# Optimization experiments

Measured on AMD Instinct MI355X. Metric: run time of the kernel, lower is better.

The kernel has to match this reference:

```python
import jax, jax.numpy as jnp
import numpy as np

N_NODES = 50000
N_EDGES = 800000
N_GRAPHS = 512
HEADS = 4
HDIM = 64
NEG_SLOPE = 0.2


def setup_inputs() -> dict:
    key = jax.random.key(0)
    ks = jax.random.split(key, 16)
    x = jax.random.normal(ks[0], (N_NODES, 128), dtype=jnp.float32)
    edge_index = jax.random.randint(ks[1], (2, N_EDGES), 0, N_NODES, dtype=jnp.int64)
    batch = jnp.sort(jax.random.randint(ks[2], (N_NODES,), 0, N_GRAPHS, dtype=jnp.int64))
    def glorot(k, shape):
        fan = shape[0] + shape[-1]
        return jax.random.normal(k, shape, dtype=jnp.float32) * jnp.sqrt(2.0 / fan)
    return {
        "x": x, "edge_index": edge_index, "batch": batch,
        "W1": glorot(ks[3], (128, 256)), "a_src1": glorot(ks[4], (HEADS, HDIM)), "a_dst1": glorot(ks[5], (HEADS, HDIM)), "b1": jnp.zeros((256,), jnp.float32),
        "W2": glorot(ks[6], (256, 256)), "a_src2": glorot(ks[7], (HEADS, HDIM)), "a_dst2": glorot(ks[8], (HEADS, HDIM)), "b2": jnp.zeros((256,), jnp.float32),
        "W3": glorot(ks[9], (256, 256)), "a_src3": glorot(ks[10], (HEADS, HDIM)), "a_dst3": glorot(ks[11], (HEADS, HDIM)), "b3": jnp.zeros((256,), jnp.float32),
        "fc_W": glorot(ks[12], (256, 1)), "fc_b": jnp.zeros((1,), jnp.float32),
    }


def gat_layer(x, W, a_src, a_dst, b, src, dst):
    # x: [N, F_in] -> h: [N, H, C]
    N = x.shape[0]
    h = (x @ W).reshape(N, HEADS, HDIM)
    alpha_s = jnp.sum(h * a_src[None], axis=-1)  # [N, H]
    alpha_d = jnp.sum(h * a_dst[None], axis=-1)  # [N, H]
    logits = jax.nn.leaky_relu(alpha_s[src] + alpha_d[dst], NEG_SLOPE)  # [E, H]
    # segment softmax over destination nodes
    m = jax.ops.segment_max(logits, dst, num_segments=N)  # [N, H]
    e = jnp.exp(logits - m[dst])
    denom = jax.ops.segment_sum(e, dst, num_segments=N)
    alpha = e / denom[dst]  # [E, H]
    msg = h[src] * alpha[:, :, None]  # [E, H, C]
    out = jax.ops.segment_sum(msg, dst, num_segments=N).reshape(N, HEADS * HDIM)
    return out + b


def reference(x, edge_index, batch, W1, a_src1, a_dst1, b1, W2, a_src2, a_dst2, b2, W3, a_src3, a_dst3, b3, fc_W, fc_b):
    N = x.shape[0]
    loop = jnp.arange(N, dtype=edge_index.dtype)
    # PyG GATConv adds self-loops by default
    src = jnp.concatenate([edge_index[0], loop])
    dst = jnp.concatenate([edge_index[1], loop])
    h = gat_layer(x, W1, a_src1, a_dst1, b1, src, dst)
    h = gat_layer(h, W2, a_src2, a_dst2, b2, src, dst)
    h = gat_layer(h, W3, a_src3, a_dst3, b3, src, dst)
    pooled = jax.ops.segment_sum(h, batch, num_segments=N_GRAPHS)  # [G, 256]
    return pooled @ fc_W + fc_b
```

## Files before the change

### kernel.cpp

```cpp
#include <hip/hip_runtime.h>
#include <hip/hip_bf16.h>
#include <math.h>

#define NN 50000
#define NE 800000
#define ET (NE + NN)
#define NG 512
#define NEG 0.2f

typedef __attribute__((ext_vector_type(8))) short bf16x8;
typedef __attribute__((ext_vector_type(4))) float f32x4;

__device__ inline unsigned f2o(float f) {
    unsigned b = __float_as_uint(f);
    return (b & 0x80000000u) ? ~b : (b | 0x80000000u);
}
__device__ inline float o2f(unsigned u) {
    return (u & 0x80000000u) ? __uint_as_float(u ^ 0x80000000u) : __uint_as_float(~u);
}
__device__ inline unsigned short f2b(float f) {
    unsigned u = __float_as_uint(f);
    u += 0x7fffu + ((u >> 16) & 1u);
    return (unsigned short)(u >> 16);
}
__device__ inline float b2f(unsigned short b) {
    return __uint_as_float(((unsigned)b) << 16);
}

__global__ __launch_bounds__(256) void split_weights(const float* __restrict__ W1,
        const float* __restrict__ W2, const float* __restrict__ W3,
        unsigned short* __restrict__ WTh, unsigned short* __restrict__ WTl) {
    int tid = blockIdx.x * 256 + threadIdx.x;
    const float* W; int K, n, k, base;
    if (tid < 32768)       { W = W1; K = 128; base = 0;     int i = tid;          n = i >> 7; k = i & 127; }
    else if (tid < 98304)  { W = W2; K = 256; base = 32768; int i = tid - 32768;  n = i >> 8; k = i & 255; }
    else if (tid < 163840) { W = W3; K = 256; base = 98304; int i = tid - 98304;  n = i >> 8; k = i & 255; }
    else return;
    float w = W[k * 256 + n];
    unsigned short hi = f2b(w);
    float lo = w - b2f(hi);
    WTh[base + n * K + k] = hi;
    WTl[base + n * K + k] = f2b(lo);
}

template<int K, int AFP32>
__global__ __launch_bounds__(256) void gemm_mfma(const float* __restrict__ Af,
        const unsigned short* __restrict__ Ahi, const unsigned short* __restrict__ Alo,
        const unsigned short* __restrict__ Bhi, const unsigned short* __restrict__ Blo,
        unsigned short* __restrict__ h,
        const float* __restrict__ a_src, const float* __restrict__ a_dst,
        float* __restrict__ as_, float* __restrict__ ad_) {
    __shared__ unsigned short AsH[128][40], AsL[128][40], BsH[128][40], BsL[128][40];
    const int t = threadIdx.x;
    const int mb = blockIdx.x >> 1, nb = blockIdx.x & 1;
    const int m0 = mb * 128, n0 = nb * 128;
    const int wid = t >> 6, lane = t & 63;
    const int wr = wid >> 1, wc = wid & 1;
    const int lr = lane & 15, lg = lane >> 4;

    f32x4 acc[4][4];
    #pragma unroll
    for (int mi = 0; mi < 4; ++mi)
        #pragma unroll
        for (int ni = 0; ni < 4; ++ni)
            acc[mi][ni] = (f32x4){0.f, 0.f, 0.f, 0.f};

    for (int k0 = 0; k0 < K; k0 += 32) {
        __syncthreads();
        #pragma unroll
        for (int cc = 0; cc < 2; ++cc) {
            int c = t + cc * 256;
            int row = c >> 2, kc = c & 3;
            int gr = m0 + row; if (gr >= NN) gr = NN - 1;
            if (AFP32) {
                const float* pa = Af + (size_t)gr * K + k0 + kc * 8;
                float4 f0 = *(const float4*)pa;
                float4 f1 = *(const float4*)(pa + 4);
                union { unsigned short u[8]; uint4 v; } th, tl;
                float fs[8] = {f0.x, f0.y, f0.z, f0.w, f1.x, f1.y, f1.z, f1.w};
                #pragma unroll
                for (int j = 0; j < 8; ++j) {
                    unsigned short hv = f2b(fs[j]);
                    th.u[j] = hv;
                    tl.u[j] = f2b(fs[j] - b2f(hv));
                }
                *(uint4*)&AsH[row][kc * 8] = th.v;
                *(uint4*)&AsL[row][kc * 8] = tl.v;
            } else {
                *(uint4*)&AsH[row][kc * 8] = *(const uint4*)(Ahi + (size_t)gr * K + k0 + kc * 8);
                *(uint4*)&AsL[row][kc * 8] = *(const uint4*)(Alo + (size_t)gr * K + k0 + kc * 8);
            }
            *(uint4*)&BsH[row][kc * 8] = *(const uint4*)(Bhi + (size_t)(n0 + row) * K + k0 + kc * 8);
            *(uint4*)&BsL[row][kc * 8] = *(const uint4*)(Blo + (size_t)(n0 + row) * K + k0 + kc * 8);
        }
        __syncthreads();

        bf16x8 ah[4], al[4];
        #pragma unroll
        for (int mi = 0; mi < 4; ++mi) {
            int ra = wr * 64 + mi * 16 + lr;
            ah[mi] = *(const bf16x8*)&AsH[ra][lg * 8];
            al[mi] = *(const bf16x8*)&AsL[ra][lg * 8];
        }
        #pragma unroll
        for (int ni = 0; ni < 4; ++ni) {
            int rb = wc * 64 + ni * 16 + lr;
            bf16x8 bh = *(const bf16x8*)&BsH[rb][lg * 8];
            bf16x8 bl = *(const bf16x8*)&BsL[rb][lg * 8];
            #pragma unroll
            for (int mi = 0; mi < 4; ++mi) {
                acc[mi][ni] = __builtin_amdgcn_mfma_f32_16x16x32_bf16(bh, ah[mi], acc[mi][ni], 0, 0, 0);
                acc[mi][ni] = __builtin_amdgcn_mfma_f32_16x16x32_bf16(bh, al[mi], acc[mi][ni], 0, 0, 0);
                acc[mi][ni] = __builtin_amdgcn_mfma_f32_16x16x32_bf16(bl, ah[mi], acc[mi][ni], 0, 0, 0);
            }
        }
    }

    const int head = nb * 2 + wc;
    const int ncol0 = n0 + wc * 64;
    float4 asv[4], adv[4];
    #pragma unroll
    for (int ni = 0; ni < 4; ++ni) {
        asv[ni] = *(const float4*)&a_src[head * 64 + ni * 16 + lg * 4];
        adv[ni] = *(const float4*)&a_dst[head * 64 + ni * 16 + lg * 4];
    }
    #pragma unroll
    for (int mi = 0; mi < 4; ++mi) {
        float ps = 0.f, pd = 0.f;
        #pragma unroll
        for (int ni = 0; ni < 4; ++ni) {
            ps = fmaf(acc[mi][ni][0], asv[ni].x, ps); pd = fmaf(acc[mi][ni][0], adv[ni].x, pd);
            ps = fmaf(acc[mi][ni][1], asv[ni].y, ps); pd = fmaf(acc[mi][ni][1], adv[ni].y, pd);
            ps = fmaf(acc[mi][ni][2], asv[ni].z, ps); pd = fmaf(acc[mi][ni][2], adv[ni].z, pd);
            ps = fmaf(acc[mi][ni][3], asv[ni].w, ps); pd = fmaf(acc[mi][ni][3], adv[ni].w, pd);
        }
        ps += __shfl_xor(ps, 16, 64); ps += __shfl_xor(ps, 32, 64);
        pd += __shfl_xor(pd, 16, 64); pd += __shfl_xor(pd, 32, 64);
        int row = m0 + wr * 64 + mi * 16 + lr;
        if (row < NN) {
            #pragma unroll
            for (int ni = 0; ni < 4; ++ni) {
                ushort4 hv = {f2b(acc[mi][ni][0]), f2b(acc[mi][ni][1]),
                              f2b(acc[mi][ni][2]), f2b(acc[mi][ni][3])};
                *(ushort4*)&h[(size_t)row * 256 + ncol0 + ni * 16 + lg * 4] = hv;
            }
            if (lane < 16) { as_[row * 4 + head] = ps; ad_[row * 4 + head] = pd; }
        }
    }
}

__global__ void gmax_init(unsigned* gmax) {
    if (threadIdx.x < 4) gmax[threadIdx.x] = 0u;
}
__global__ __launch_bounds__(256) void gmax_reduce(const float* __restrict__ as_,
                                                   unsigned* gmax) {
    float m0 = -1e30f, m1 = -1e30f, m2 = -1e30f, m3 = -1e30f;
    for (int n = blockIdx.x * 256 + threadIdx.x; n < NN; n += gridDim.x * 256) {
        float4 a = *(const float4*)&as_[n * 4];
        m0 = fmaxf(m0, a.x); m1 = fmaxf(m1, a.y);
        m2 = fmaxf(m2, a.z); m3 = fmaxf(m3, a.w);
    }
    #pragma unroll
    for (int off = 32; off; off >>= 1) {
        m0 = fmaxf(m0, __shfl_xor(m0, off, 64));
        m1 = fmaxf(m1, __shfl_xor(m1, off, 64));
        m2 = fmaxf(m2, __shfl_xor(m2, off, 64));
        m3 = fmaxf(m3, __shfl_xor(m3, off, 64));
    }
    __shared__ float sm[4][4];
    int lane = threadIdx.x & 63, w = threadIdx.x >> 6;
    if (lane == 0) { sm[w][0] = m0; sm[w][1] = m1; sm[w][2] = m2; sm[w][3] = m3; }
    __syncthreads();
    if (threadIdx.x == 0) {
        #pragma unroll
        for (int hd = 0; hd < 4; ++hd) {
            float mm = fmaxf(fmaxf(sm[0][hd], sm[1][hd]), fmaxf(sm[2][hd], sm[3][hd]));
            atomicMax(&gmax[hd], f2o(mm));
        }
    }
}

__global__ void init_counts(int* counts, int* esrc_pad) {
    int i = blockIdx.x * 256 + threadIdx.x;
    if (i < NN) counts[i] = 1;
    if (i < 24) esrc_pad[i] = 0;
}
__global__ void count_kernel(const int* __restrict__ dst, int* counts) {
    int e = blockIdx.x * 256 + threadIdx.x;
    if (e < NE) atomicAdd(&counts[dst[e]], 1);
}
__global__ __launch_bounds__(1024) void scan_kernel(const int* __restrict__ counts,
                                                    int* row_ptr, int* cursor) {
    __shared__ int sm[1024];
    const int i = threadIdx.x;
    const int CH = (NN + 1023) / 1024;
    int base = i * CH;
    int s = 0;
    for (int j = 0; j < CH; ++j) { int idx = base + j; if (idx < NN) s += counts[idx]; }
    sm[i] = s; __syncthreads();
    for (int off = 1; off < 1024; off <<= 1) {
        int v = (i >= off) ? sm[i - off] : 0;
        __syncthreads();
        sm[i] += v;
        __syncthreads();
    }
    int run = sm[i] - s;
    for (int j = 0; j < CH; ++j) {
        int idx = base + j;
        if (idx < NN) { row_ptr[idx] = run; cursor[idx] = run; run += counts[idx]; }
    }
    if (i == 1023) row_ptr[NN] = ET;
}
__global__ void scatter_kernel(const int* __restrict__ src, const int* __restrict__ dst,
                               int* cursor, int* esrc) {
    int e = blockIdx.x * 256 + threadIdx.x;
    if (e < NE) {
        int p = atomicAdd(&cursor[dst[e]], 1);
        esrc[p] = src[e];
    } else if (e < ET) {
        int n = e - NE;
        int p = atomicAdd(&cursor[n], 1);
        esrc[p] = n;
    }
}

#define EDGE(ae, he)                                                           \
    {                                                                          \
        float t_ = (ae) + adn; t_ = t_ > 0.f ? t_ : NEG * t_;                  \
        float w_ = __expf(t_ - g); lsum += w_;                                 \
        acc.x = fmaf(w_, b2f((he).x), acc.x);                                  \
        acc.y = fmaf(w_, b2f((he).y), acc.y);                                  \
        acc.z = fmaf(w_, b2f((he).z), acc.z);                                  \
        acc.w = fmaf(w_, b2f((he).w), acc.w);                                  \
    }

template<int FINAL>
__global__ __launch_bounds__(256) void agg_kernel(const unsigned short* __restrict__ h,
        const float* __restrict__ as_, const float* __restrict__ ad_,
        const unsigned* __restrict__ gmax,
        const int* __restrict__ row_ptr, const int* __restrict__ esrc,
        const float* __restrict__ bias,
        unsigned short* __restrict__ ohi, unsigned short* __restrict__ olo,
        float* __restrict__ out,
        const int* __restrict__ batch, const float* __restrict__ fcW) {
    int n = blockIdx.x * 4 + (threadIdx.x >> 6);
    int lane = threadIdx.x & 63;
    if (n >= NN) return;
    const int head = lane >> 4;
    const int c4 = lane * 4;
    int s0 = row_ptr[n], s1 = row_ptr[n + 1];
    float adn = ad_[n * 4 + head];
    float g = o2f(gmax[head]) + adn; g = g > 0.f ? g : NEG * g;
    float lsum = 0.f;
    float4 acc = {0.f, 0.f, 0.f, 0.f};

    int i = s0;
    int iA[8], iB[8];
    #pragma unroll
    for (int j = 0; j < 8; ++j) iA[j] = esrc[i + j];
    #pragma unroll
    for (int j = 0; j < 8; ++j) iB[j] = esrc[i + 8 + j];
    float aA[8]; ushort4 hA[8];
    #pragma unroll
    for (int j = 0; j < 8; ++j) aA[j] = as_[iA[j] * 4 + head];
    #pragma unroll
    for (int j = 0; j < 8; ++j) hA[j] = *(const ushort4*)&h[(long)iA[j] * 256 + c4];

    while (i + 8 < s1) {
        int iC[8];
        #pragma unroll
        for (int j = 0; j < 8; ++j) iC[j] = esrc[i + 16 + j];
        float aB[8]; ushort4 hB[8];
        #pragma unroll
        for (int j = 0; j < 8; ++j) aB[j] = as_[iB[j] * 4 + head];
        #pragma unroll
        for (int j = 0; j < 8; ++j) hB[j] = *(const ushort4*)&h[(long)iB[j] * 256 + c4];
        #pragma unroll
        for (int j = 0; j < 8; ++j) EDGE(aA[j], hA[j]);
        #pragma unroll
        for (int j = 0; j < 8; ++j) { iB[j] = iC[j]; aA[j] = aB[j]; hA[j] = hB[j]; }
        i += 8;
    }
    #pragma unroll
    for (int j = 0; j < 8; ++j) {
        float t_ = aA[j] + adn; t_ = t_ > 0.f ? t_ : NEG * t_;
        float w_ = (i + j < s1) ? __expf(t_ - g) : 0.f;
        lsum += w_;
        acc.x = fmaf(w_, b2f(hA[j].x), acc.x);
        acc.y = fmaf(w_, b2f(hA[j].y), acc.y);
        acc.z = fmaf(w_, b2f(hA[j].z), acc.z);
        acc.w = fmaf(w_, b2f(hA[j].w), acc.w);
    }

    float rl = 1.f / lsum;
    float4 bv = *(const float4*)&bias[c4];
    float4 o = {fmaf(acc.x, rl, bv.x), fmaf(acc.y, rl, bv.y),
                fmaf(acc.z, rl, bv.z), fmaf(acc.w, rl, bv.w)};
    if (!FINAL) {
        ushort4 vh = {f2b(o.x), f2b(o.y), f2b(o.z), f2b(o.w)};
        ushort4 vl = {f2b(o.x - b2f(vh.x)), f2b(o.y - b2f(vh.y)),
                      f2b(o.z - b2f(vh.z)), f2b(o.w - b2f(vh.w))};
        *(ushort4*)&ohi[(long)n * 256 + c4] = vh;
        *(ushort4*)&olo[(long)n * 256 + c4] = vl;
    } else {
        float4 fw = *(const float4*)&fcW[c4];
        float sd = o.x * fw.x + o.y * fw.y + o.z * fw.z + o.w * fw.w;
        #pragma unroll
        for (int off = 32; off; off >>= 1) sd += __shfl_xor(sd, off, 64);
        if (lane == 0) atomicAdd(&out[batch[n]], sd);
    }
}

__global__ void out_init(const float* __restrict__ fc_b, float* out) {
    int i = blockIdx.x * 256 + threadIdx.x;
    if (i < NG) out[i] = fc_b[0];
}

extern "C" void kernel_launch(void* const* d_in, const int* in_sizes, int n_in,
                              void* d_out, int out_size, void* d_ws, size_t ws_size,
                              hipStream_t stream) {
    const float* x      = (const float*)d_in[0];
    const int*   ei     = (const int*)d_in[1];
    const int*   batch  = (const int*)d_in[2];
    const float* W1     = (const float*)d_in[3];
    const float* as1    = (const float*)d_in[4];
    const float* ad1    = (const float*)d_in[5];
    const float* b1     = (const float*)d_in[6];
    const float* W2     = (const float*)d_in[7];
    const float* as2    = (const float*)d_in[8];
    const float* ad2    = (const float*)d_in[9];
    const float* b2     = (const float*)d_in[10];
    const float* W3     = (const float*)d_in[11];
    const float* as3    = (const float*)d_in[12];
    const float* ad3    = (const float*)d_in[13];
    const float* b3     = (const float*)d_in[14];
    const float* fcW    = (const float*)d_in[15];
    const float* fcb    = (const float*)d_in[16];
    const int* esrc_in = ei;
    const int* edst_in = ei + NE;

    char* ws = (char*)d_ws;
    size_t off = 0;
    unsigned short* hB  = (unsigned short*)(ws + off); off += (size_t)NN * 256 * 2;
    unsigned short* ohi = (unsigned short*)(ws + off); off += (size_t)NN * 256 * 2;
    unsigned short* olo = (unsigned short*)(ws + off); off += (size_t)NN * 256 * 2;
    unsigned short* WTh = (unsigned short*)(ws + off); off += 163840 * 2;
    unsigned short* WTl = (unsigned short*)(ws + off); off += 163840 * 2;
    float* aS    = (float*)(ws + off); off += (size_t)NN * 4 * 4;
    float* aD    = (float*)(ws + off); off += (size_t)NN * 4 * 4;
    int* counts  = (int*)(ws + off);   off += (size_t)NN * 4;
    int* cursor  = (int*)(ws + off);   off += (size_t)NN * 4;
    int* row_ptr = (int*)(ws + off);   off += (size_t)(NN + 1) * 4 + 12;
    unsigned* gmax = (unsigned*)(ws + off); off += 16;
    int* esrc    = (int*)(ws + off);   off += (size_t)(ET + 24) * 4;
    float* out   = (float*)d_out;

    init_counts<<<(NN + 255) / 256, 256, 0, stream>>>(counts, esrc + ET);
    count_kernel<<<(NE + 255) / 256, 256, 0, stream>>>(edst_in, counts);
    scan_kernel<<<1, 1024, 0, stream>>>(counts, row_ptr, cursor);
    scatter_kernel<<<(ET + 255) / 256, 256, 0, stream>>>(esrc_in, edst_in, cursor, esrc);
    split_weights<<<640, 256, 0, stream>>>(W1, W2, W3, WTh, WTl);

    const int GEMM_GRID = ((NN + 127) / 128) * 2;
    const int NODE_GRID = (NN + 3) / 4;

    gmax_init<<<1, 64, 0, stream>>>(gmax);
    gemm_mfma<128, 1><<<GEMM_GRID, 256, 0, stream>>>(x, nullptr, nullptr, WTh, WTl, hB, as1, ad1, aS, aD);
    gmax_reduce<<<128, 256, 0, stream>>>(aS, gmax);
    agg_kernel<0><<<NODE_GRID, 256, 0, stream>>>(hB, aS, aD, gmax, row_ptr, esrc, b1, ohi, olo, nullptr, nullptr, nullptr);
    gmax_init<<<1, 64, 0, stream>>>(gmax);
    gemm_mfma<256, 0><<<GEMM_GRID, 256, 0, stream>>>(nullptr, ohi, olo, WTh + 32768, WTl + 32768, hB, as2, ad2, aS, aD);
    gmax_reduce<<<128, 256, 0, stream>>>(aS, gmax);
    agg_kernel<0><<<NODE_GRID, 256, 0, stream>>>(hB, aS, aD, gmax, row_ptr, esrc, b2, ohi, olo, nullptr, nullptr, nullptr);
    gmax_init<<<1, 64, 0, stream>>>(gmax);
    gemm_mfma<256, 0><<<GEMM_GRID, 256, 0, stream>>>(nullptr, ohi, olo, WTh + 98304, WTl + 98304, hB, as3, ad3, aS, aD);
    gmax_reduce<<<128, 256, 0, stream>>>(aS, gmax);
    out_init<<<(NG + 255) / 256, 256, 0, stream>>>(fcb, out);
    agg_kernel<1><<<NODE_GRID, 256, 0, stream>>>(hB, aS, aD, gmax, row_ptr, esrc, b3, nullptr, nullptr, out, batch, fcW);
}
```

Before: 640.7 us.

## Fuse global attention max into GEMM epilogue and re-pipeline edge gather

The per-head global max of the source attention scores is now computed inside the GEMM epilogue, using wave shuffles and one atomicMax per wave. The three gmax_init and three gmax_reduce launches are removed, and the buffers are zeroed once in init_counts with a separate slot per layer. The aggregation kernel's gather pipeline changes from an 8-wide triple-buffered scheme to two 4-wide double-buffered groups, which lowers register pressure and adds a tail path for the leftover edges. The cost is extra atomic traffic in the GEMM and a more complex remainder handling in the aggregation loop.

```diff
diff --git a/kernel.cpp b/kernel.cpp
--- a/kernel.cpp
+++ b/kernel.cpp
@@ -49,7 +49,8 @@
         const unsigned short* __restrict__ Bhi, const unsigned short* __restrict__ Blo,
         unsigned short* __restrict__ h,
         const float* __restrict__ a_src, const float* __restrict__ a_dst,
-        float* __restrict__ as_, float* __restrict__ ad_) {
+        float* __restrict__ as_, float* __restrict__ ad_,
+        unsigned* __restrict__ gmax) {
     __shared__ unsigned short AsH[128][40], AsL[128][40], BsH[128][40], BsL[128][40];
     const int t = threadIdx.x;
     const int mb = blockIdx.x >> 1, nb = blockIdx.x & 1;
@@ -124,6 +125,7 @@
         asv[ni] = *(const float4*)&a_src[head * 64 + ni * 16 + lg * 4];
         adv[ni] = *(const float4*)&a_dst[head * 64 + ni * 16 + lg * 4];
     }
+    float pmax = -1e30f;
     #pragma unroll
     for (int mi = 0; mi < 4; ++mi) {
         float ps = 0.f, pd = 0.f;
@@ -136,6 +138,7 @@
         }
         ps += __shfl_xor(ps, 16, 64); ps += __shfl_xor(ps, 32, 64);
         pd += __shfl_xor(pd, 16, 64); pd += __shfl_xor(pd, 32, 64);
+        pmax = fmaxf(pmax, ps);
         int row = m0 + wr * 64 + mi * 16 + lr;
         if (row < NN) {
             #pragma unroll
@@ -147,43 +150,18 @@
             if (lane < 16) { as_[row * 4 + head] = ps; ad_[row * 4 + head] = pd; }
         }
     }
-}
-
-__global__ void gmax_init(unsigned* gmax) {
-    if (threadIdx.x < 4) gmax[threadIdx.x] = 0u;
-}
-__global__ __launch_bounds__(256) void gmax_reduce(const float* __restrict__ as_,
-                                                   unsigned* gmax) {
-    float m0 = -1e30f, m1 = -1e30f, m2 = -1e30f, m3 = -1e30f;
-    for (int n = blockIdx.x * 256 + threadIdx.x; n < NN; n += gridDim.x * 256) {
-        float4 a = *(const float4*)&as_[n * 4];
-        m0 = fmaxf(m0, a.x); m1 = fmaxf(m1, a.y);
-        m2 = fmaxf(m2, a.z); m3 = fmaxf(m3, a.w);
-    }
-    #pragma unroll
-    for (int off = 32; off; off >>= 1) {
-        m0 = fmaxf(m0, __shfl_xor(m0, off, 64));
-        m1 = fmaxf(m1, __shfl_xor(m1, off, 64));
-        m2 = fmaxf(m2, __shfl_xor(m2, off, 64));
-        m3 = fmaxf(m3, __shfl_xor(m3, off, 64));
-    }
-    __shared__ float sm[4][4];
-    int lane = threadIdx.x & 63, w = threadIdx.x >> 6;
-    if (lane == 0) { sm[w][0] = m0; sm[w][1] = m1; sm[w][2] = m2; sm[w][3] = m3; }
-    __syncthreads();
-    if (threadIdx.x == 0) {
-        #pragma unroll
-        for (int hd = 0; hd < 4; ++hd) {
-            float mm = fmaxf(fmaxf(sm[0][hd], sm[1][hd]), fmaxf(sm[2][hd], sm[3][hd]));
-            atomicMax(&gmax[hd], f2o(mm));
-        }
-    }
-}
-
-__global__ void init_counts(int* counts, int* esrc_pad) {
+    pmax = fmaxf(pmax, __shfl_xor(pmax, 1, 64));
+    pmax = fmaxf(pmax, __shfl_xor(pmax, 2, 64));
+    pmax = fmaxf(pmax, __shfl_xor(pmax, 4, 64));
+    pmax = fmaxf(pmax, __shfl_xor(pmax, 8, 64));
+    if (lane == 0) atomicMax(&gmax[head], f2o(pmax));
+}
+
+__global__ void init_counts(int* counts, int* esrc_pad, unsigned* gmax) {
     int i = blockIdx.x * 256 + threadIdx.x;
     if (i < NN) counts[i] = 1;
     if (i < 24) esrc_pad[i] = 0;
+    if (i < 12) gmax[i] = 0u;
 }
 __global__ void count_kernel(const int* __restrict__ dst, int* counts) {
     int e = blockIdx.x * 256 + threadIdx.x;
@@ -255,41 +233,71 @@
     float4 acc = {0.f, 0.f, 0.f, 0.f};
 
     int i = s0;
-    int iA[8], iB[8];
-    #pragma unroll
-    for (int j = 0; j < 8; ++j) iA[j] = esrc[i + j];
-    #pragma unroll
-    for (int j = 0; j < 8; ++j) iB[j] = esrc[i + 8 + j];
-    float aA[8]; ushort4 hA[8];
-    #pragma unroll
-    for (int j = 0; j < 8; ++j) aA[j] = as_[iA[j] * 4 + head];
-    #pragma unroll
-    for (int j = 0; j < 8; ++j) hA[j] = *(const ushort4*)&h[(long)iA[j] * 256 + c4];
-
-    while (i + 8 < s1) {
-        int iC[8];
-        #pragma unroll
-        for (int j = 0; j < 8; ++j) iC[j] = esrc[i + 16 + j];
-        float aB[8]; ushort4 hB[8];
-        #pragma unroll
-        for (int j = 0; j < 8; ++j) aB[j] = as_[iB[j] * 4 + head];
-        #pragma unroll
-        for (int j = 0; j < 8; ++j) hB[j] = *(const ushort4*)&h[(long)iB[j] * 256 + c4];
-        #pragma unroll
-        for (int j = 0; j < 8; ++j) EDGE(aA[j], hA[j]);
-        #pragma unroll
-        for (int j = 0; j < 8; ++j) { iB[j] = iC[j]; aA[j] = aB[j]; hA[j] = hB[j]; }
+    int iC[4], iD[4];
+    float aA[4], aB[4]; ushort4 hA[4], hB[4];
+    {
+        int iA[4], iB[4];
+        #pragma unroll
+        for (int j = 0; j < 4; ++j) iA[j] = esrc[i + j];
+        #pragma unroll
+        for (int j = 0; j < 4; ++j) iB[j] = esrc[i + 4 + j];
+        #pragma unroll
+        for (int j = 0; j < 4; ++j) { aA[j] = as_[iA[j] * 4 + head]; hA[j] = *(const ushort4*)&h[(long)iA[j] * 256 + c4]; }
+        #pragma unroll
+        for (int j = 0; j < 4; ++j) { aB[j] = as_[iB[j] * 4 + head]; hB[j] = *(const ushort4*)&h[(long)iB[j] * 256 + c4]; }
+        #pragma unroll
+        for (int j = 0; j < 4; ++j) iC[j] = esrc[i + 8 + j];
+        #pragma unroll
+        for (int j = 0; j < 4; ++j) iD[j] = esrc[i + 12 + j];
+    }
+
+    while (i + 16 <= s1) {
+        #pragma unroll
+        for (int j = 0; j < 4; ++j) EDGE(aA[j], hA[j]);
+        #pragma unroll
+        for (int j = 0; j < 4; ++j) { aA[j] = as_[iC[j] * 4 + head]; hA[j] = *(const ushort4*)&h[(long)iC[j] * 256 + c4]; }
+        #pragma unroll
+        for (int j = 0; j < 4; ++j) iC[j] = esrc[i + 16 + j];
+        #pragma unroll
+        for (int j = 0; j < 4; ++j) EDGE(aB[j], hB[j]);
+        #pragma unroll
+        for (int j = 0; j < 4; ++j) { aB[j] = as_[iD[j] * 4 + head]; hB[j] = *(const ushort4*)&h[(long)iD[j] * 256 + c4]; }
+        #pragma unroll
+        for (int j = 0; j < 4; ++j) iD[j] = esrc[i + 20 + j];
         i += 8;
     }
-    #pragma unroll
-    for (int j = 0; j < 8; ++j) {
+
+    int r = s1 - i;
+    if (r > 8) {
+        #pragma unroll
+        for (int j = 0; j < 4; ++j) EDGE(aA[j], hA[j]);
+        #pragma unroll
+        for (int j = 0; j < 4; ++j) EDGE(aB[j], hB[j]);
+        #pragma unroll
+        for (int j = 0; j < 4; ++j) { aA[j] = as_[iC[j] * 4 + head]; hA[j] = *(const ushort4*)&h[(long)iC[j] * 256 + c4]; }
+        #pragma unroll
+        for (int j = 0; j < 4; ++j) { aB[j] = as_[iD[j] * 4 + head]; hB[j] = *(const ushort4*)&h[(long)iD[j] * 256 + c4]; }
+        r -= 8;
+    }
+    #pragma unroll
+    for (int j = 0; j < 4; ++j) {
         float t_ = aA[j] + adn; t_ = t_ > 0.f ? t_ : NEG * t_;
-        float w_ = (i + j < s1) ? __expf(t_ - g) : 0.f;
+        float w_ = (j < r) ? __expf(t_ - g) : 0.f;
         lsum += w_;
         acc.x = fmaf(w_, b2f(hA[j].x), acc.x);
         acc.y = fmaf(w_, b2f(hA[j].y), acc.y);
         acc.z = fmaf(w_, b2f(hA[j].z), acc.z);
         acc.w = fmaf(w_, b2f(hA[j].w), acc.w);
+    }
+    #pragma unroll
+    for (int j = 0; j < 4; ++j) {
+        float t_ = aB[j] + adn; t_ = t_ > 0.f ? t_ : NEG * t_;
+        float w_ = (4 + j < r) ? __expf(t_ - g) : 0.f;
+        lsum += w_;
+        acc.x = fmaf(w_, b2f(hB[j].x), acc.x);
+        acc.y = fmaf(w_, b2f(hB[j].y), acc.y);
+        acc.z = fmaf(w_, b2f(hB[j].z), acc.z);
+        acc.w = fmaf(w_, b2f(hB[j].w), acc.w);
     }
 
     float rl = 1.f / lsum;
@@ -351,11 +359,11 @@
     int* counts  = (int*)(ws + off);   off += (size_t)NN * 4;
     int* cursor  = (int*)(ws + off);   off += (size_t)NN * 4;
     int* row_ptr = (int*)(ws + off);   off += (size_t)(NN + 1) * 4 + 12;
-    unsigned* gmax = (unsigned*)(ws + off); off += 16;
+    unsigned* gmax = (unsigned*)(ws + off); off += 48;
     int* esrc    = (int*)(ws + off);   off += (size_t)(ET + 24) * 4;
     float* out   = (float*)d_out;
 
-    init_counts<<<(NN + 255) / 256, 256, 0, stream>>>(counts, esrc + ET);
+    init_counts<<<(NN + 255) / 256, 256, 0, stream>>>(counts, esrc + ET, gmax);
     count_kernel<<<(NE + 255) / 256, 256, 0, stream>>>(edst_in, counts);
     scan_kernel<<<1, 1024, 0, stream>>>(counts, row_ptr, cursor);
     scatter_kernel<<<(ET + 255) / 256, 256, 0, stream>>>(esrc_in, edst_in, cursor, esrc);
@@ -364,17 +372,11 @@
     const int GEMM_GRID = ((NN + 127) / 128) * 2;
     const int NODE_GRID = (NN + 3) / 4;
 
-    gmax_init<<<1, 64, 0, stream>>>(gmax);
-    gemm_mfma<128, 1><<<GEMM_GRID, 256, 0, stream>>>(x, nullptr, nullptr, WTh, WTl, hB, as1, ad1, aS, aD);
-    gmax_reduce<<<128, 256, 0, stream>>>(aS, gmax);
+    gemm_mfma<128, 1><<<GEMM_GRID, 256, 0, stream>>>(x, nullptr, nullptr, WTh, WTl, hB, as1, ad1, aS, aD, gmax);
     agg_kernel<0><<<NODE_GRID, 256, 0, stream>>>(hB, aS, aD, gmax, row_ptr, esrc, b1, ohi, olo, nullptr, nullptr, nullptr);
-    gmax_init<<<1, 64, 0, stream>>>(gmax);
-    gemm_mfma<256, 0><<<GEMM_GRID, 256, 0, stream>>>(nullptr, ohi, olo, WTh + 32768, WTl + 32768, hB, as2, ad2, aS, aD);
-    gmax_reduce<<<128, 256, 0, stream>>>(aS, gmax);
-    agg_kernel<0><<<NODE_GRID, 256, 0, stream>>>(hB, aS, aD, gmax, row_ptr, esrc, b2, ohi, olo, nullptr, nullptr, nullptr);
-    gmax_init<<<1, 64, 0, stream>>>(gmax);
-    gemm_mfma<256, 0><<<GEMM_GRID, 256, 0, stream>>>(nullptr, ohi, olo, WTh + 98304, WTl + 98304, hB, as3, ad3, aS, aD);
-    gmax_reduce<<<128, 256, 0, stream>>>(aS, gmax);
+    gemm_mfma<256, 0><<<GEMM_GRID, 256, 0, stream>>>(nullptr, ohi, olo, WTh + 32768, WTl + 32768, hB, as2, ad2, aS, aD, gmax + 4);
+    agg_kernel<0><<<NODE_GRID, 256, 0, stream>>>(hB, aS, aD, gmax + 4, row_ptr, esrc, b2, ohi, olo, nullptr, nullptr, nullptr);
+    gemm_mfma<256, 0><<<GEMM_GRID, 256, 0, stream>>>(nullptr, ohi, olo, WTh + 98304, WTl + 98304, hB, as3, ad3, aS, aD, gmax + 8);
     out_init<<<(NG + 255) / 256, 256, 0, stream>>>(fcb, out);
-    agg_kernel<1><<<NODE_GRID, 256, 0, stream>>>(hB, aS, aD, gmax, row_ptr, esrc, b3, nullptr, nullptr, out, batch, fcW);
-}
+    agg_kernel<1><<<NODE_GRID, 256, 0, stream>>>(hB, aS, aD, gmax + 8, row_ptr, esrc, b3, nullptr, nullptr, out, batch, fcW);
+}
```

Result: slower. 668.1 us (+4.3%).
